# Kernel tuning notes

Hardware: AMD Instinct MI355X
Metric: run time of the kernel (lower is better)

## Reference

```python
import jax, jax.numpy as jnp
import numpy as np

N, E, G = 50000, 800000, 512          # nodes, edges, graphs in batch
DIN, DH, H, DOUT = 128, 128, 2, 128   # dim_in, dim_h, heads, dim_out
NEG_SLOPE = 0.2
EPS_BN = 1e-5


def setup_inputs():
    key = jax.random.key(0)
    ks = jax.random.split(key, 12)
    def glorot(k, shape, fan):
        return (jax.random.normal(k, shape, jnp.float32) / np.float32(np.sqrt(fan)))
    return dict(
        x=jax.random.normal(ks[0], (N, DIN), jnp.float32),
        edge_index=jax.random.randint(ks[1], (2, E), 0, N, dtype=jnp.int32),
        batch=jnp.sort(jax.random.randint(ks[2], (N,), 0, G, dtype=jnp.int32)),
        Wl1=glorot(ks[3], (DIN, H * DH), DIN),
        Wr1=glorot(ks[4], (DIN, H * DH), DIN),
        att1=glorot(ks[5], (H, DH), DH),
        b1=jnp.zeros((H * DH,), jnp.float32),
        gamma=jnp.ones((H * DH,), jnp.float32),
        beta=jnp.zeros((H * DH,), jnp.float32),
        Wl2=glorot(ks[6], (H * DH, DOUT), H * DH),
        Wr2=glorot(ks[7], (H * DH, DOUT), H * DH),
        att2=glorot(ks[8], (1, DOUT), DOUT),
        b2=jnp.zeros((DOUT,), jnp.float32),
        Wlin=glorot(ks[9], (DOUT, 2), DOUT),
        blin=jnp.zeros((2,), jnp.float32),
    )


def gatv2_conv(x, src, dst, Wl, Wr, att, bias, heads, dh, n):
    # x: [n, F]; src/dst: [Etot] (self-loops already appended)
    xl = (x @ Wl).reshape(n, heads, dh)  # source transform (messages)
    xr = (x @ Wr).reshape(n, heads, dh)  # target transform
    m = xl[src] + xr[dst]                             # [Etot, H, dh]
    e = jnp.einsum('ehd,hd->eh', jax.nn.leaky_relu(m, NEG_SLOPE), att)  # [Etot, H]
    # softmax over incoming edges of each target node
    emax = jax.ops.segment_max(e, dst, num_segments=n)
    ex = jnp.exp(e - emax[dst])
    denom = jax.ops.segment_sum(ex, dst, num_segments=n)
    alpha = ex / (denom[dst] + 1e-16)                 # [Etot, H]
    out = jax.ops.segment_sum(xl[src] * alpha[:, :, None], dst, num_segments=n)
    return out.reshape(n, heads * dh) + bias


def reference(x, edge_index, batch, Wl1, Wr1, att1, b1, gamma, beta,
              Wl2, Wr2, att2, b2, Wlin, blin):
    loops = jnp.arange(N, dtype=edge_index.dtype)
    src = jnp.concatenate([edge_index[0], loops])
    dst = jnp.concatenate([edge_index[1], loops])

    h = gatv2_conv(x, src, dst, Wl1, Wr1, att1, b1, H, DH, N)   # [N, H*DH]
    h = jax.nn.elu(h)
    # BatchNorm over node dimension (training-mode batch stats)
    mu = h.mean(axis=0)
    var = h.var(axis=0)
    h = (h - mu) * jax.lax.rsqrt(var + EPS_BN) * gamma + beta
    # dropout p=0 -> identity
    h = gatv2_conv(h, src, dst, Wl2, Wr2, att2, b2, 1, DOUT, N)  # [N, DOUT]

    # global mean pool per graph
    s = jax.ops.segment_sum(h, batch, num_segments=G)
    cnt = jax.ops.segment_sum(jnp.ones((N,), h.dtype), batch, num_segments=G)
    pooled = s / jnp.maximum(cnt, 1.0)[:, None]                  # [G, DOUT]
    return pooled @ Wlin + blin                                  # [G, 2]
```

## Files before the change

kernel.cpp:

```cpp
#include <hip/hip_runtime.h>


#define DIN 128
#define F1 256
#define F2 128
#define NEG_SLOPE 0.2f

typedef unsigned short u16;
typedef __attribute__((ext_vector_type(8))) short short8;
typedef __attribute__((ext_vector_type(4))) float floatx4;
typedef __attribute__((ext_vector_type(2))) float f32x2;

__device__ __forceinline__ float bf2f(u16 u) {
  return __uint_as_float(((unsigned int)u) << 16);
}
__device__ __forceinline__ u16 f2bf(float f) {
  unsigned int x = __float_as_uint(f);
  return (u16)((x + 0x7fffu + ((x >> 16) & 1u)) >> 16);
}
__device__ __forceinline__ void load8(const u16* p, float (&f)[8]) {
  short8 v = *(const short8*)p;
#pragma unroll
  for (int k = 0; k < 8; k++) f[k] = bf2f((u16)v[k]);
}

__device__ __forceinline__ f32x2 bf2x(unsigned int u) {
  f32x2 r;
  r.x = __uint_as_float(u << 16);
  r.y = __uint_as_float(u & 0xffff0000u);
  return r;
}
__device__ __forceinline__ f32x2 pk_add(f32x2 a, f32x2 b) {
  f32x2 d;
  asm("v_pk_add_f32 %0, %1, %2" : "=v"(d) : "v"(a), "v"(b));
  return d;
}
__device__ __forceinline__ f32x2 pk_fma(f32x2 a, f32x2 b, f32x2 c) {
  f32x2 d;
  asm("v_pk_fma_f32 %0, %1, %2, %3" : "=v"(d) : "v"(a), "v"(b), "v"(c));
  return d;
}
__device__ __forceinline__ f32x2 pk_abs(f32x2 a) {
  f32x2 r;
  r.x = __uint_as_float(__float_as_uint(a.x) & 0x7fffffffu);
  r.y = __uint_as_float(__float_as_uint(a.y) & 0x7fffffffu);
  return r;
}

template <int CTRL>
__device__ __forceinline__ float dppadd(float s) {
  int t = __builtin_amdgcn_update_dpp(0, __float_as_int(s), CTRL, 0xF, 0xF, false);
  return s + __int_as_float(t);
}

struct PTab { const void* src[8]; int off[9]; };
__global__ __launch_bounds__(256) void k_convert_all(
    const void* __restrict__ xsrc, u16* __restrict__ xb, int n4, int nxb,
    PTab t, u16* __restrict__ pb, int ptotal, int npb,
    const void* __restrict__ Wl1s, const void* __restrict__ Wr1s,
    const void* __restrict__ Wl2s, const void* __restrict__ Wr2s,
    u16* __restrict__ Wl1t, u16* __restrict__ Wr1t,
    u16* __restrict__ Wl2t, u16* __restrict__ Wr2t,
    int* __restrict__ zbase, int zn, int* __restrict__ flag) {
  __shared__ int flagS;
  int tid = threadIdx.x;
  if (tid < 64) {
    int cnt = 0;
#pragma unroll
    for (int i = 0; i < 2; ++i) {
      u16 v = ((const u16*)xsrc)[2 * (tid + 64 * i)];
      int e = (v >> 7) & 0xFF;
      if (e >= 115 && e <= 130) cnt++;
    }
#pragma unroll
    for (int m = 1; m <= 32; m <<= 1) cnt += __shfl_xor(cnt, m, 64);
    if (tid == 0) flagS = (cnt < 64) ? 1 : 0;
  }
  __syncthreads();
  const int fl = flagS;
  if (blockIdx.x == 0 && tid == 0) *flag = fl;

  int b = blockIdx.x;
  if (b < nxb) {
    int i = b * 256 + tid;
    if (i >= n4) return;
    if (fl) {
      float4 a = ((const float4*)xsrc)[i];
      ushort4 o;
      o.x = f2bf(a.x); o.y = f2bf(a.y); o.z = f2bf(a.z); o.w = f2bf(a.w);
      ((ushort4*)xb)[i] = o;
    } else {
      ((ulong1*)xb)[i] = ((const ulong1*)xsrc)[i];
    }
    return;
  }
  b -= nxb;
  if (b < npb) {
    int i = b * 256 + tid;
    if (i >= ptotal) return;
    int s = 0;
#pragma unroll
    for (int k = 1; k < 8; k++) s += (i >= t.off[k]);
    int local = i - t.off[s];
    pb[i] = fl ? f2bf(((const float*)t.src[s])[local]) : ((const u16*)t.src[s])[local];
    return;
  }
  b -= npb;
  if (b < 512) {
    int seg = b >> 7;
    int i = (b & 127) * 256 + tid;
    const void* s; u16* d; int NL, sh;
    if      (seg == 0) { s = Wl1s; d = Wl1t; NL = 256; sh = 7; }
    else if (seg == 1) { s = Wr1s; d = Wr1t; NL = 256; sh = 7; }
    else if (seg == 2) { s = Wl2s; d = Wl2t; NL = 128; sh = 8; }
    else               { s = Wr2s; d = Wr2t; NL = 128; sh = 8; }
    int n = i >> sh, k = i & ((1 << sh) - 1);
    int si = k * NL + n;
    d[i] = fl ? f2bf(((const float*)s)[si]) : ((const u16*)s)[si];
    return;
  }
  b -= 512;
  int i = b * 256 + tid;
  if (i < zn) zbase[i] = 0;
}

__global__ void k_hist(const int* __restrict__ ei, int* __restrict__ hist,
                       int E, int Etot) {
  int e = blockIdx.x * 256 + threadIdx.x;
  if (e >= Etot) return;
  int dst = (e < E) ? ei[E + e] : (e - E);
  atomicAdd(&hist[dst], 1);
}

__global__ void k_scan(const int* __restrict__ hist, int* __restrict__ rowptr,
                       int* __restrict__ cursor, unsigned long long* __restrict__ pstate,
                       int* __restrict__ ctr, int n, int Etot) {
  __shared__ int tmp[256];
  __shared__ int bidS, offS;
  int t = threadIdx.x;
  if (t == 0) bidS = atomicAdd(ctr, 1);
  __syncthreads();
  int bid = bidS;
  int gid = bid * 256 + t;
  int v = (gid < n) ? hist[gid] : 0;
  tmp[t] = v;
  __syncthreads();
  for (int off = 1; off < 256; off <<= 1) {
    int add = (t >= off) ? tmp[t - off] : 0;
    __syncthreads();
    tmp[t] += add;
    __syncthreads();
  }
  if (t == 0) {
    int total = tmp[255];
    unsigned long long st =
        ((unsigned long long)(bid == 0 ? 2 : 1) << 32) | (unsigned)total;
    atomicExch(&pstate[bid], st);
    int off = 0;
    if (bid > 0) {
      int b = bid - 1;
      while (true) {
        unsigned long long s;
        do { s = atomicAdd(&pstate[b], 0ULL); } while ((s >> 32) == 0);
        off += (int)(unsigned)s;
        if ((s >> 32) == 2) break;
        b--;
      }
      atomicExch(&pstate[bid],
                 ((unsigned long long)2 << 32) | (unsigned)(off + total));
    }
    offS = off;
  }
  __syncthreads();
  int off = offS;
  if (gid < n) {
    int ex = off + tmp[t] - v;
    rowptr[gid] = ex;
    cursor[gid] = ex;
  }
  if (gid == 0) rowptr[n] = Etot;
}

__global__ void k_scatter(const int* __restrict__ ei, int* __restrict__ cursor,
                          int* __restrict__ ssrc, int E, int Etot) {
  int e = blockIdx.x * 256 + threadIdx.x;
  if (e >= Etot) return;
  int src, dst;
  if (e < E) { src = ei[e]; dst = ei[E + e]; }
  else       { src = e - E; dst = e - E; }
  int pos = atomicAdd(&cursor[dst], 1);
  ssrc[pos] = src;
}

template<int K, bool RB>
__global__ __launch_bounds__(256) void k_gemm(
    const u16* __restrict__ A, const u16* __restrict__ Blt, const u16* __restrict__ Brt,
    int NL, u16* __restrict__ Cl, u16* __restrict__ Cr, int M,
    const float* __restrict__ rbias) {
  const int tid = threadIdx.x;
  const int m0 = blockIdx.x * 64;
  const int n0g = blockIdx.y * 64;
  const u16* Bt; u16* C; int col0;
  if (n0g < NL) { Bt = Blt; C = Cl; col0 = n0g; }
  else          { Bt = Brt; C = Cr; col0 = n0g - NL; }

  const int wave = tid >> 6, lane = tid & 63;
  const int wm = wave >> 1, wn = wave & 1;
  const int quad = lane >> 4, l16 = lane & 15;

  floatx4 acc[2][2] = {};
#pragma unroll
  for (int k0 = 0; k0 < K; k0 += 32) {
    short8 af[2], bfr[2];
#pragma unroll
    for (int mt = 0; mt < 2; mt++) {
      int row = m0 + wm * 32 + mt * 16 + l16;
      if (row > M - 1) row = M - 1;
      af[mt] = *(const short8*)(A + (size_t)row * K + k0 + quad * 8);
    }
#pragma unroll
    for (int nt = 0; nt < 2; nt++) {
      int nn = col0 + wn * 32 + nt * 16 + l16;
      bfr[nt] = *(const short8*)(Bt + (size_t)nn * K + k0 + quad * 8);
    }
#pragma unroll
    for (int mt = 0; mt < 2; mt++)
#pragma unroll
      for (int nt = 0; nt < 2; nt++)
        acc[mt][nt] = __builtin_amdgcn_mfma_f32_16x16x32_bf16(af[mt], bfr[nt], acc[mt][nt], 0, 0, 0);
  }

#pragma unroll
  for (int mt = 0; mt < 2; mt++)
#pragma unroll
    for (int nt = 0; nt < 2; nt++) {
      float rb = 0.f;
      if (RB) rb = rbias[n0g + wn * 32 + nt * 16 + l16];
#pragma unroll
      for (int r = 0; r < 4; r++) {
        int row = m0 + wm * 32 + mt * 16 + quad * 4 + r;
        if (row < M) {
          int col = col0 + wn * 32 + nt * 16 + l16;
          C[(size_t)row * NL + col] = f2bf(acc[mt][nt][r] + rb);
        }
      }
    }
}

template<int CPL, int MODE>
__global__ __launch_bounds__(256) void k_agg(
    const u16* __restrict__ xl, const u16* __restrict__ xr,
    const u16* __restrict__ att, const u16* __restrict__ bias,
    const int* __restrict__ rowptr, const int* __restrict__ ssrc,
    void* __restrict__ outv, int n) {
  constexpr int F = CPL * 16;
  constexpr int NV = CPL / 8;
  constexpr int NP = CPL / 2;
  int wave = threadIdx.x >> 6, lane = threadIdx.x & 63;
  int node = blockIdx.x * 4 + wave;
  if (node >= n) return;
  const int q = lane >> 4, l = lane & 15;
  const int ch0 = l * CPL;

  f32x2 xr2[NP], a06[NP], acc2[NP];
  {
    const unsigned int* xru = (const unsigned int*)(xr + (size_t)node * F + ch0);
    const unsigned int* atu = (const unsigned int*)(att + ch0);
#pragma unroll
    for (int p = 0; p < NP; p++) {
      xr2[p] = bf2x(xru[p]);
      f32x2 a = bf2x(atu[p]);
      a06[p].x = 0.6f * a.x; a06[p].y = 0.6f * a.y;
      acc2[p].x = 0.f;       acc2[p].y = 0.f;
    }
  }
  f32x2 c23; c23.x = 2.0f / 3.0f; c23.y = 2.0f / 3.0f;

  const int jb = __builtin_amdgcn_readfirstlane(rowptr[node]);
  const int je = __builtin_amdgcn_readfirstlane(rowptr[node + 1]);
  const int jec = je - 1;
  float l_run = 0.f;

  auto cidx = [&](int j) -> int { return j < jec ? j : jec; };

  uint4 bufA[NV], bufB[NV];
  auto REFILL = [&](uint4 (&buf)[NV], int srow) {
#pragma unroll
    for (int v = 0; v < NV; v++)
      buf[v] = *(const uint4*)(xl + (size_t)srow * F + ch0 + v * 8);
  };

  auto SLOT = [&](uint4 (&buf)[NV], int jbase) {
    f32x2 xl2[NP];
    f32x2 s2; s2.x = 0.f; s2.y = 0.f;
#pragma unroll
    for (int v = 0; v < NV; v++) {
      unsigned int dw[4] = {buf[v].x, buf[v].y, buf[v].z, buf[v].w};
#pragma unroll
      for (int k = 0; k < 4; k++) {
        const int p = v * 4 + k;
        f32x2 xv = bf2x(dw[k]);
        f32x2 m  = pk_add(xv, xr2[p]);
        f32x2 am = pk_abs(m);
        f32x2 t  = pk_fma(am, c23, m);
        s2 = pk_fma(a06[p], t, s2);
        xl2[p] = xv;
      }
    }
    float s = s2.x + s2.y;
    s = dppadd<0xB1>(s);
    s = dppadd<0x4E>(s);
    s = dppadd<0x141>(s);
    if (CPL == 8) s = dppadd<0x140>(s);
    float pe = (jbase + q < je) ? __expf(fminf(s, 80.f)) : 0.f;
    l_run += pe;
    f32x2 p2; p2.x = pe; p2.y = pe;
#pragma unroll
    for (int p = 0; p < NP; p++) acc2[p] = pk_fma(p2, xl2[p], acc2[p]);
  };

  REFILL(bufA, ssrc[cidx(jb + q)]);
  REFILL(bufB, ssrc[cidx(jb + 4 + q)]);
  int sA2 = ssrc[cidx(jb + 8 + q)];
  int sB2 = ssrc[cidx(jb + 12 + q)];

  int j = jb;
  for (; j + 4 < je; j += 8) {
    SLOT(bufA, j);
    REFILL(bufA, sA2);
    SLOT(bufB, j + 4);
    REFILL(bufB, sB2);
    sA2 = ssrc[cidx(j + 16 + q)];
    sB2 = ssrc[cidx(j + 20 + q)];
  }
  if (j < je) SLOT(bufA, j);

#pragma unroll
  for (int p = 0; p < NP; p++) {
    acc2[p].x += __shfl_xor(acc2[p].x, 16, 64);
    acc2[p].x += __shfl_xor(acc2[p].x, 32, 64);
    acc2[p].y += __shfl_xor(acc2[p].y, 16, 64);
    acc2[p].y += __shfl_xor(acc2[p].y, 32, 64);
  }
  l_run += __shfl_xor(l_run, 16, 64);
  l_run += __shfl_xor(l_run, 32, 64);

  if (q == 0) {
    float inv = 1.f / (l_run + 1e-16f);
    const unsigned int* bu = (const unsigned int*)(bias + ch0);
    if (MODE == 0) {
#pragma unroll
      for (int v = 0; v < NV; v++) {
        short8 o;
#pragma unroll
        for (int k = 0; k < 4; k++) {
          const int p = v * 4 + k;
          f32x2 b = bf2x(bu[p]);
          float t0 = acc2[p].x * inv + b.x;
          float t1 = acc2[p].y * inv + b.y;
          t0 = t0 > 0.f ? t0 : (__expf(t0) - 1.f);
          t1 = t1 > 0.f ? t1 : (__expf(t1) - 1.f);
          o[k * 2]     = (short)f2bf(t0);
          o[k * 2 + 1] = (short)f2bf(t1);
        }
        *(short8*)((u16*)outv + (size_t)node * F + ch0 + v * 8) = o;
      }
    } else {
#pragma unroll
      for (int v = 0; v < NV; v++) {
        float w[8];
#pragma unroll
        for (int k = 0; k < 4; k++) {
          const int p = v * 4 + k;
          f32x2 b = bf2x(bu[p]);
          w[k * 2]     = acc2[p].x * inv + b.x;
          w[k * 2 + 1] = acc2[p].y * inv + b.y;
        }
        float* op = (float*)outv + (size_t)node * F + ch0 + v * 8;
        *(float4*)op = make_float4(w[0], w[1], w[2], w[3]);
        *(float4*)(op + 4) = make_float4(w[4], w[5], w[6], w[7]);
      }
    }
  }
}

__global__ __launch_bounds__(256) void k_stats(
    const u16* __restrict__ h, float* __restrict__ gsum,
    float* __restrict__ gsumsq, int n) {
  __shared__ float smS[8][256], smQ[8][256];
  int t = threadIdx.x;
  int rg = t >> 5, cl = t & 31;
  int ch0 = cl * 8;
  float s[8] = {}, q[8] = {};
  for (int r = blockIdx.x * 8 + rg; r < n; r += gridDim.x * 8) {
    float v[8];
    load8(h + (size_t)r * F1 + ch0, v);
#pragma unroll
    for (int k = 0; k < 8; k++) { s[k] += v[k]; q[k] += v[k] * v[k]; }
  }
#pragma unroll
  for (int k = 0; k < 8; k++) { smS[rg][ch0 + k] = s[k]; smQ[rg][ch0 + k] = q[k]; }
  __syncthreads();
  float ts = 0.f, tq = 0.f;
#pragma unroll
  for (int g = 0; g < 8; g++) { ts += smS[g][t]; tq += smQ[g][t]; }
  atomicAdd(&gsum[t], ts);
  atomicAdd(&gsumsq[t], tq);
}

__global__ __launch_bounds__(256) void k_foldbn(
    const float* __restrict__ gsum, const float* __restrict__ gsumsq,
    const u16* __restrict__ gamma, const u16* __restrict__ beta,
    u16* __restrict__ Wl2t, u16* __restrict__ Wr2t,
    float* __restrict__ rbias, float invn) {
  __shared__ float red[8];
  int t = threadIdx.x, n = blockIdx.x;
  float mu = gsum[t] * invn;
  float var = gsumsq[t] * invn - mu * mu;
  float a = bf2f(gamma[t]) * rsqrtf(fmaxf(var, 0.f) + 1e-5f);
  float b = bf2f(beta[t]) - mu * a;
  float wl = bf2f(Wl2t[n * 256 + t]);
  float wr = bf2f(Wr2t[n * 256 + t]);
  float sl = b * wl, sr = b * wr;
  Wl2t[n * 256 + t] = f2bf(a * wl);
  Wr2t[n * 256 + t] = f2bf(a * wr);
#pragma unroll
  for (int m = 1; m <= 32; m <<= 1) {
    sl += __shfl_xor(sl, m, 64);
    sr += __shfl_xor(sr, m, 64);
  }
  int wave = t >> 6, lane = t & 63;
  if (lane == 0) { red[wave] = sl; red[4 + wave] = sr; }
  __syncthreads();
  if (t == 0) rbias[n] = red[0] + red[1] + red[2] + red[3];
  if (t == 1) rbias[128 + n] = red[4] + red[5] + red[6] + red[7];
}

__device__ __forceinline__ int lowerb(const int* __restrict__ a, int n, int key) {
  int lo = 0, hi = n;
  while (lo < hi) { int m = (lo + hi) >> 1; if (a[m] < key) lo = m + 1; else hi = m; }
  return lo;
}

__global__ __launch_bounds__(256) void k_poolfinal(
    const float* __restrict__ h2, const int* __restrict__ batch,
    const u16* __restrict__ Wlin, const u16* __restrict__ blin,
    void* __restrict__ out, const int* __restrict__ flag, int G, int N) {
  __shared__ float sm[4][128];
  int g = blockIdx.x;
  int wave = threadIdx.x >> 6, lane = threadIdx.x & 63;
  int jb = lowerb(batch, N, g);
  int je = lowerb(batch, N, g + 1);
  int ch = lane * 2;
  float c0 = 0.f, c1 = 0.f;
  for (int r = jb + wave; r < je; r += 4) {
    float2 v = *(const float2*)(h2 + (size_t)r * F2 + ch);
    c0 += v.x; c1 += v.y;
  }
  sm[wave][ch] = c0;
  sm[wave][ch + 1] = c1;
  __syncthreads();
  if (wave == 0) {
    c0 = sm[0][ch] + sm[1][ch] + sm[2][ch] + sm[3][ch];
    c1 = sm[0][ch + 1] + sm[1][ch + 1] + sm[2][ch + 1] + sm[3][ch + 1];
    float cf = fmaxf((float)(je - jb), 1.f);
    c0 /= cf; c1 /= cf;
    float s0 = c0 * bf2f(Wlin[ch * 2 + 0]) + c1 * bf2f(Wlin[(ch + 1) * 2 + 0]);
    float s1 = c0 * bf2f(Wlin[ch * 2 + 1]) + c1 * bf2f(Wlin[(ch + 1) * 2 + 1]);
#pragma unroll
    for (int m = 1; m <= 32; m <<= 1) {
      s0 += __shfl_xor(s0, m, 64);
      s1 += __shfl_xor(s1, m, 64);
    }
    if (lane == 0) {
      float o0 = s0 + bf2f(blin[0]);
      float o1 = s1 + bf2f(blin[1]);
      if (*flag) {
        ((float*)out)[g * 2 + 0] = o0;
        ((float*)out)[g * 2 + 1] = o1;
      } else {
        ((u16*)out)[g * 2 + 0] = f2bf(o0);
        ((u16*)out)[g * 2 + 1] = f2bf(o1);
      }
    }
  }
}

extern "C" void kernel_launch(void* const* d_in, const int* in_sizes, int n_in,
                              void* d_out, int out_size, void* d_ws, size_t ws_size,
                              hipStream_t stream) {
  const int* ei    = (const int*)d_in[1];
  const int* batch = (const int*)d_in[2];

  const int N = in_sizes[0] / DIN;
  const int E = in_sizes[1] / 2;
  const int G = out_size / 2;
  const int Etot = E + N;

  char* p = (char*)d_ws;
  auto alloc = [&](size_t bytes) {
    char* r = p;
    p += (bytes + 255) & ~(size_t)255;
    return r;
  };
  int*  flag     = (int*)alloc(256);
  int*  hist     = (int*)alloc((size_t)N * 4);
  float* gsum    = (float*)alloc(1024);
  float* gsumsq  = (float*)alloc(1024);
  unsigned long long* pstate = (unsigned long long*)alloc(2048);
  int*  ctr      = (int*)alloc(256);
  int   zn       = (int)(((char*)ctr + 256) - (char*)hist) / 4;
  int*  rowptr   = (int*)alloc((size_t)(N + 1) * 4);
  int*  cursor   = (int*)alloc((size_t)N * 4);
  float* rbias   = (float*)alloc(256 * 4);
  int*  ssrc     = (int*)alloc((size_t)Etot * 4);
  u16*  xb       = (u16*)alloc((size_t)N * DIN * 2);
  u16*  pb       = (u16*)alloc(4096);
  u16*  Wl1t     = (u16*)alloc(DIN * F1 * 2);
  u16*  Wr1t     = (u16*)alloc(DIN * F1 * 2);
  u16*  Wl2t     = (u16*)alloc(F1 * F2 * 2);
  u16*  Wr2t     = (u16*)alloc(F1 * F2 * 2);
  u16*  regionA  = (u16*)alloc((size_t)N * F1 * 2);
  u16*  regionB  = (u16*)alloc((size_t)N * F1 * 2);
  u16*  regionC  = (u16*)alloc((size_t)N * F1 * 2);

  u16*  xl1  = regionA;
  u16*  xr1  = regionB;
  u16*  helu = regionC;
  u16*  xl2  = regionB;
  u16*  xr2  = regionB + (size_t)N * F2;
  float* h2  = (float*)regionA;

  const int pidx[8] = {5, 6, 7, 8, 11, 12, 13, 14};
  PTab tab;
  int accum = 0;
  for (int i = 0; i < 8; i++) {
    tab.src[i] = d_in[pidx[i]];
    tab.off[i] = accum;
    accum += in_sizes[pidx[i]];
  }
  tab.off[8] = accum;
  int n4 = in_sizes[0] / 4;
  int nxb = (n4 + 255) / 256;
  int npb = (accum + 255) / 256;
  int nzb = (zn + 255) / 256;
  k_convert_all<<<nxb + npb + 512 + nzb, 256, 0, stream>>>(
      d_in[0], xb, n4, nxb, tab, pb, accum, npb,
      d_in[3], d_in[4], d_in[9], d_in[10], Wl1t, Wr1t, Wl2t, Wr2t,
      hist, zn, flag);
  u16 *pAtt1 = pb + tab.off[0], *pB1 = pb + tab.off[1], *pGamma = pb + tab.off[2],
      *pBeta = pb + tab.off[3], *pAtt2 = pb + tab.off[4], *pB2 = pb + tab.off[5],
      *pWlin = pb + tab.off[6], *pBlin = pb + tab.off[7];

  const int eb = (Etot + 255) / 256;
  const int sb = (N + 255) / 256;

  k_hist<<<eb, 256, 0, stream>>>(ei, hist, E, Etot);
  k_scan<<<sb, 256, 0, stream>>>(hist, rowptr, cursor, pstate, ctr, N, Etot);
  k_scatter<<<eb, 256, 0, stream>>>(ei, cursor, ssrc, E, Etot);

  dim3 g1((N + 63) / 64, (2 * F1) / 64);
  k_gemm<DIN, false><<<g1, 256, 0, stream>>>(xb, Wl1t, Wr1t, F1, xl1, xr1, N, nullptr);

  k_agg<16, 0><<<(N + 3) / 4, 256, 0, stream>>>(xl1, xr1, pAtt1, pB1, rowptr, ssrc, helu, N);

  k_stats<<<256, 256, 0, stream>>>(helu, gsum, gsumsq, N);
  k_foldbn<<<128, 256, 0, stream>>>(gsum, gsumsq, pGamma, pBeta, Wl2t, Wr2t, rbias,
                                    1.0f / (float)N);

  dim3 g2((N + 63) / 64, (2 * F2) / 64);
  k_gemm<F1, true><<<g2, 256, 0, stream>>>(helu, Wl2t, Wr2t, F2, xl2, xr2, N, rbias);

  k_agg<8, 1><<<(N + 3) / 4, 256, 0, stream>>>(xl2, xr2, pAtt2, pB2, rowptr, ssrc, h2, N);

  k_poolfinal<<<G, 256, 0, stream>>>(h2, batch, pWlin, pBlin, d_out, flag, G, N);
}
```

Measured before the change: 434.7 us.

## Make GAT aggregation kernels persistent with atomic per-wave node scheduling

```diff
diff --git a/kernel.cpp b/kernel.cpp
--- a/kernel.cpp
+++ b/kernel.cpp
@@ -248,137 +248,149 @@
 }
 
 template<int CPL, int MODE>
-__global__ __launch_bounds__(256) void k_agg(
+__global__ __launch_bounds__(256, 8) void k_agg(
     const u16* __restrict__ xl, const u16* __restrict__ xr,
     const u16* __restrict__ att, const u16* __restrict__ bias,
     const int* __restrict__ rowptr, const int* __restrict__ ssrc,
-    void* __restrict__ outv, int n) {
+    void* __restrict__ outv, int* __restrict__ wctr, int n) {
   constexpr int F = CPL * 16;
   constexpr int NV = CPL / 8;
   constexpr int NP = CPL / 2;
-  int wave = threadIdx.x >> 6, lane = threadIdx.x & 63;
-  int node = blockIdx.x * 4 + wave;
-  if (node >= n) return;
+  const int lane = threadIdx.x & 63;
   const int q = lane >> 4, l = lane & 15;
   const int ch0 = l * CPL;
 
-  f32x2 xr2[NP], a06[NP], acc2[NP];
+  f32x2 a06[NP];
   {
-    const unsigned int* xru = (const unsigned int*)(xr + (size_t)node * F + ch0);
     const unsigned int* atu = (const unsigned int*)(att + ch0);
 #pragma unroll
     for (int p = 0; p < NP; p++) {
-      xr2[p] = bf2x(xru[p]);
       f32x2 a = bf2x(atu[p]);
       a06[p].x = 0.6f * a.x; a06[p].y = 0.6f * a.y;
-      acc2[p].x = 0.f;       acc2[p].y = 0.f;
     }
   }
   f32x2 c23; c23.x = 2.0f / 3.0f; c23.y = 2.0f / 3.0f;
 
-  const int jb = __builtin_amdgcn_readfirstlane(rowptr[node]);
-  const int je = __builtin_amdgcn_readfirstlane(rowptr[node + 1]);
-  const int jec = je - 1;
-  float l_run = 0.f;
-
-  auto cidx = [&](int j) -> int { return j < jec ? j : jec; };
-
-  uint4 bufA[NV], bufB[NV];
-  auto REFILL = [&](uint4 (&buf)[NV], int srow) {
-#pragma unroll
-    for (int v = 0; v < NV; v++)
-      buf[v] = *(const uint4*)(xl + (size_t)srow * F + ch0 + v * 8);
-  };
-
-  auto SLOT = [&](uint4 (&buf)[NV], int jbase) {
-    f32x2 xl2[NP];
-    f32x2 s2; s2.x = 0.f; s2.y = 0.f;
-#pragma unroll
-    for (int v = 0; v < NV; v++) {
-      unsigned int dw[4] = {buf[v].x, buf[v].y, buf[v].z, buf[v].w};
-#pragma unroll
-      for (int k = 0; k < 4; k++) {
-        const int p = v * 4 + k;
-        f32x2 xv = bf2x(dw[k]);
-        f32x2 m  = pk_add(xv, xr2[p]);
-        f32x2 am = pk_abs(m);
-        f32x2 t  = pk_fma(am, c23, m);
-        s2 = pk_fma(a06[p], t, s2);
-        xl2[p] = xv;
+  for (;;) {
+    int ndv = 0;
+    if (lane == 0) ndv = atomicAdd(wctr, 1);
+    const int node = __builtin_amdgcn_readfirstlane(ndv);
+    if (node >= n) return;
+
+    f32x2 xr2[NP], acc2[NP];
+    {
+      const unsigned int* xru = (const unsigned int*)(xr + (size_t)node * F + ch0);
+#pragma unroll
+      for (int p = 0; p < NP; p++) {
+        xr2[p] = bf2x(xru[p]);
+        acc2[p].x = 0.f; acc2[p].y = 0.f;
       }
     }
-    float s = s2.x + s2.y;
-    s = dppadd<0xB1>(s);
-    s = dppadd<0x4E>(s);
-    s = dppadd<0x141>(s);
-    if (CPL == 8) s = dppadd<0x140>(s);
-    float pe = (jbase + q < je) ? __expf(fminf(s, 80.f)) : 0.f;
-    l_run += pe;
-    f32x2 p2; p2.x = pe; p2.y = pe;
-#pragma unroll
-    for (int p = 0; p < NP; p++) acc2[p] = pk_fma(p2, xl2[p], acc2[p]);
-  };
-
-  REFILL(bufA, ssrc[cidx(jb + q)]);
-  REFILL(bufB, ssrc[cidx(jb + 4 + q)]);
-  int sA2 = ssrc[cidx(jb + 8 + q)];
-  int sB2 = ssrc[cidx(jb + 12 + q)];
-
-  int j = jb;
-  for (; j + 4 < je; j += 8) {
-    SLOT(bufA, j);
-    REFILL(bufA, sA2);
-    SLOT(bufB, j + 4);
-    REFILL(bufB, sB2);
-    sA2 = ssrc[cidx(j + 16 + q)];
-    sB2 = ssrc[cidx(j + 20 + q)];
-  }
-  if (j < je) SLOT(bufA, j);
-
-#pragma unroll
-  for (int p = 0; p < NP; p++) {
-    acc2[p].x += __shfl_xor(acc2[p].x, 16, 64);
-    acc2[p].x += __shfl_xor(acc2[p].x, 32, 64);
-    acc2[p].y += __shfl_xor(acc2[p].y, 16, 64);
-    acc2[p].y += __shfl_xor(acc2[p].y, 32, 64);
-  }
-  l_run += __shfl_xor(l_run, 16, 64);
-  l_run += __shfl_xor(l_run, 32, 64);
-
-  if (q == 0) {
-    float inv = 1.f / (l_run + 1e-16f);
-    const unsigned int* bu = (const unsigned int*)(bias + ch0);
-    if (MODE == 0) {
+
+    const int jb = __builtin_amdgcn_readfirstlane(rowptr[node]);
+    const int je = __builtin_amdgcn_readfirstlane(rowptr[node + 1]);
+    const int jec = je - 1;
+    float l_run = 0.f;
+
+    auto cidx = [&](int j) -> int { return j < jec ? j : jec; };
+
+    uint4 bufA[NV], bufB[NV];
+    auto REFILL = [&](uint4 (&buf)[NV], int srow) {
+#pragma unroll
+      for (int v = 0; v < NV; v++)
+        buf[v] = *(const uint4*)(xl + (size_t)srow * F + ch0 + v * 8);
+    };
+
+    auto SLOT = [&](uint4 (&buf)[NV], int jbase) {
+      f32x2 xl2[NP];
+      f32x2 s2; s2.x = 0.f; s2.y = 0.f;
 #pragma unroll
       for (int v = 0; v < NV; v++) {
-        short8 o;
+        unsigned int dw[4] = {buf[v].x, buf[v].y, buf[v].z, buf[v].w};
 #pragma unroll
         for (int k = 0; k < 4; k++) {
           const int p = v * 4 + k;
-          f32x2 b = bf2x(bu[p]);
-          float t0 = acc2[p].x * inv + b.x;
-          float t1 = acc2[p].y * inv + b.y;
-          t0 = t0 > 0.f ? t0 : (__expf(t0) - 1.f);
-          t1 = t1 > 0.f ? t1 : (__expf(t1) - 1.f);
-          o[k * 2]     = (short)f2bf(t0);
-          o[k * 2 + 1] = (short)f2bf(t1);
+          f32x2 xv = bf2x(dw[k]);
+          f32x2 m  = pk_add(xv, xr2[p]);
+          f32x2 am = pk_abs(m);
+          f32x2 t  = pk_fma(am, c23, m);
+          s2 = pk_fma(a06[p], t, s2);
+          xl2[p] = xv;
         }
-        *(short8*)((u16*)outv + (size_t)node * F + ch0 + v * 8) = o;
       }
-    } else {
-#pragma unroll
-      for (int v = 0; v < NV; v++) {
-        float w[8];
-#pragma unroll
-        for (int k = 0; k < 4; k++) {
-          const int p = v * 4 + k;
-          f32x2 b = bf2x(bu[p]);
-          w[k * 2]     = acc2[p].x * inv + b.x;
-          w[k * 2 + 1] = acc2[p].y * inv + b.y;
+      float s = s2.x + s2.y;
+      s = dppadd<0xB1>(s);
+      s = dppadd<0x4E>(s);
+      s = dppadd<0x141>(s);
+      if (CPL == 8) s = dppadd<0x140>(s);
+      float pe = (jbase + q < je) ? __expf(fminf(s, 80.f)) : 0.f;
+      l_run += pe;
+      f32x2 p2; p2.x = pe; p2.y = pe;
+#pragma unroll
+      for (int p = 0; p < NP; p++) acc2[p] = pk_fma(p2, xl2[p], acc2[p]);
+    };
+
+    REFILL(bufA, ssrc[cidx(jb + q)]);
+    REFILL(bufB, ssrc[cidx(jb + 4 + q)]);
+    int sA2 = ssrc[cidx(jb + 8 + q)];
+    int sB2 = ssrc[cidx(jb + 12 + q)];
+
+    int j = jb;
+    for (; j + 4 < je; j += 8) {
+      SLOT(bufA, j);
+      REFILL(bufA, sA2);
+      SLOT(bufB, j + 4);
+      REFILL(bufB, sB2);
+      sA2 = ssrc[cidx(j + 16 + q)];
+      sB2 = ssrc[cidx(j + 20 + q)];
+    }
+    if (j < je) SLOT(bufA, j);
+
+#pragma unroll
+    for (int p = 0; p < NP; p++) {
+      acc2[p].x += __shfl_xor(acc2[p].x, 16, 64);
+      acc2[p].x += __shfl_xor(acc2[p].x, 32, 64);
+      acc2[p].y += __shfl_xor(acc2[p].y, 16, 64);
+      acc2[p].y += __shfl_xor(acc2[p].y, 32, 64);
+    }
+    l_run += __shfl_xor(l_run, 16, 64);
+    l_run += __shfl_xor(l_run, 32, 64);
+
+    if (q == 0) {
+      float inv = 1.f / (l_run + 1e-16f);
+      const unsigned int* bu = (const unsigned int*)(bias + ch0);
+      if (MODE == 0) {
+#pragma unroll
+        for (int v = 0; v < NV; v++) {
+          short8 o;
+#pragma unroll
+          for (int k = 0; k < 4; k++) {
+            const int p = v * 4 + k;
+            f32x2 b = bf2x(bu[p]);
+            float t0 = acc2[p].x * inv + b.x;
+            float t1 = acc2[p].y * inv + b.y;
+            t0 = t0 > 0.f ? t0 : (__expf(t0) - 1.f);
+            t1 = t1 > 0.f ? t1 : (__expf(t1) - 1.f);
+            o[k * 2]     = (short)f2bf(t0);
+            o[k * 2 + 1] = (short)f2bf(t1);
+          }
+          *(short8*)((u16*)outv + (size_t)node * F + ch0 + v * 8) = o;
         }
-        float* op = (float*)outv + (size_t)node * F + ch0 + v * 8;
-        *(float4*)op = make_float4(w[0], w[1], w[2], w[3]);
-        *(float4*)(op + 4) = make_float4(w[4], w[5], w[6], w[7]);
+      } else {
+#pragma unroll
+        for (int v = 0; v < NV; v++) {
+          float w[8];
+#pragma unroll
+          for (int k = 0; k < 4; k++) {
+            const int p = v * 4 + k;
+            f32x2 b = bf2x(bu[p]);
+            w[k * 2]     = acc2[p].x * inv + b.x;
+            w[k * 2 + 1] = acc2[p].y * inv + b.y;
+          }
+          float* op = (float*)outv + (size_t)node * F + ch0 + v * 8;
+          *(float4*)op = make_float4(w[0], w[1], w[2], w[3]);
+          *(float4*)(op + 4) = make_float4(w[4], w[5], w[6], w[7]);
+        }
       }
     }
   }
@@ -509,7 +521,8 @@
   float* gsumsq  = (float*)alloc(1024);
   unsigned long long* pstate = (unsigned long long*)alloc(2048);
   int*  ctr      = (int*)alloc(256);
-  int   zn       = (int)(((char*)ctr + 256) - (char*)hist) / 4;
+  int*  wctr     = (int*)alloc(256);
+  int   zn       = (int)(((char*)wctr + 256) - (char*)hist) / 4;
   int*  rowptr   = (int*)alloc((size_t)(N + 1) * 4);
   int*  cursor   = (int*)alloc((size_t)N * 4);
   float* rbias   = (float*)alloc(256 * 4);
@@ -562,7 +575,9 @@
   dim3 g1((N + 63) / 64, (2 * F1) / 64);
   k_gemm<DIN, false><<<g1, 256, 0, stream>>>(xb, Wl1t, Wr1t, F1, xl1, xr1, N, nullptr);
 
-  k_agg<16, 0><<<(N + 3) / 4, 256, 0, stream>>>(xl1, xr1, pAtt1, pB1, rowptr, ssrc, helu, N);
+  const int PW = 2048;
+  k_agg<16, 0><<<PW, 256, 0, stream>>>(xl1, xr1, pAtt1, pB1, rowptr, ssrc, helu,
+                                       wctr, N);
 
   k_stats<<<256, 256, 0, stream>>>(helu, gsum, gsumsq, N);
   k_foldbn<<<128, 256, 0, stream>>>(gsum, gsumsq, pGamma, pBeta, Wl2t, Wr2t, rbias,
@@ -571,7 +586,8 @@
   dim3 g2((N + 63) / 64, (2 * F2) / 64);
   k_gemm<F1, true><<<g2, 256, 0, stream>>>(helu, Wl2t, Wr2t, F2, xl2, xr2, N, rbias);
 
-  k_agg<8, 1><<<(N + 3) / 4, 256, 0, stream>>>(xl2, xr2, pAtt2, pB2, rowptr, ssrc, h2, N);
+  k_agg<8, 1><<<PW, 256, 0, stream>>>(xl2, xr2, pAtt2, pB2, rowptr, ssrc, h2,
+                                      wctr + 64, N);
 
   k_poolfinal<<<G, 256, 0, stream>>>(h2, batch, pWlin, pBlin, d_out, flag, G, N);
 }
```

Measured after the change: 1.727 ms. 3.97x slower.

## Add specialized layer-2 aggregation kernel with 8 edges per wave and double-buffered gathers

Applied to the files above, without the earlier changes.

```diff
diff --git a/kernel.cpp b/kernel.cpp
--- a/kernel.cpp
+++ b/kernel.cpp
@@ -380,6 +380,126 @@
         *(float4*)op = make_float4(w[0], w[1], w[2], w[3]);
         *(float4*)(op + 4) = make_float4(w[4], w[5], w[6], w[7]);
       }
+    }
+  }
+}
+
+__global__ __launch_bounds__(256) void k_agg2(
+    const u16* __restrict__ xl, const u16* __restrict__ xr,
+    const u16* __restrict__ att, const u16* __restrict__ bias,
+    const int* __restrict__ rowptr, const int* __restrict__ ssrc,
+    float* __restrict__ out, int n) {
+  constexpr int F = 128;
+  constexpr int NV = 2;
+  constexpr int NP = 8;
+  constexpr int GPW = 8;
+  int wave = threadIdx.x >> 6, lane = threadIdx.x & 63;
+  int node = blockIdx.x * 4 + wave;
+  if (node >= n) return;
+  const int g = lane >> 3, lg = lane & 7;
+  const int ch0 = lg * 16;
+
+  f32x2 xr2[NP], a06[NP], acc2[NP];
+  {
+    const unsigned int* xru = (const unsigned int*)(xr + (size_t)node * F + ch0);
+    const unsigned int* atu = (const unsigned int*)(att + ch0);
+#pragma unroll
+    for (int p = 0; p < NP; p++) {
+      xr2[p] = bf2x(xru[p]);
+      f32x2 a = bf2x(atu[p]);
+      a06[p].x = 0.6f * a.x; a06[p].y = 0.6f * a.y;
+      acc2[p].x = 0.f;       acc2[p].y = 0.f;
+    }
+  }
+  f32x2 c23; c23.x = 2.0f / 3.0f; c23.y = 2.0f / 3.0f;
+
+  const int jb = __builtin_amdgcn_readfirstlane(rowptr[node]);
+  const int je = __builtin_amdgcn_readfirstlane(rowptr[node + 1]);
+  const int jec = je - 1;
+  float l_run = 0.f;
+
+  auto cidx = [&](int j) -> int { return j < jec ? j : jec; };
+
+  uint4 bufA[NV], bufB[NV];
+  auto REFILL = [&](uint4 (&buf)[NV], int srow) {
+#pragma unroll
+    for (int v = 0; v < NV; v++)
+      buf[v] = *(const uint4*)(xl + (size_t)srow * F + ch0 + v * 8);
+  };
+
+  auto SLOT = [&](uint4 (&buf)[NV], int jbase) {
+    f32x2 xl2[NP];
+    f32x2 s2; s2.x = 0.f; s2.y = 0.f;
+#pragma unroll
+    for (int v = 0; v < NV; v++) {
+      unsigned int dw[4] = {buf[v].x, buf[v].y, buf[v].z, buf[v].w};
+#pragma unroll
+      for (int k = 0; k < 4; k++) {
+        const int p = v * 4 + k;
+        f32x2 xv = bf2x(dw[k]);
+        f32x2 m  = pk_add(xv, xr2[p]);
+        f32x2 am = pk_abs(m);
+        f32x2 t  = pk_fma(am, c23, m);
+        s2 = pk_fma(a06[p], t, s2);
+        xl2[p] = xv;
+      }
+    }
+    float s = s2.x + s2.y;
+    s = dppadd<0xB1>(s);
+    s = dppadd<0x4E>(s);
+    s = dppadd<0x141>(s);
+    float pe = (jbase + g < je) ? __expf(fminf(s, 80.f)) : 0.f;
+    l_run += pe;
+    f32x2 p2; p2.x = pe; p2.y = pe;
+#pragma unroll
+    for (int p = 0; p < NP; p++) acc2[p] = pk_fma(p2, xl2[p], acc2[p]);
+  };
+
+  REFILL(bufA, ssrc[cidx(jb + g)]);
+  REFILL(bufB, ssrc[cidx(jb + GPW + g)]);
+  int sA2 = ssrc[cidx(jb + 2 * GPW + g)];
+  int sB2 = ssrc[cidx(jb + 3 * GPW + g)];
+
+  int j = jb;
+  for (; j + GPW < je; j += 2 * GPW) {
+    SLOT(bufA, j);
+    REFILL(bufA, sA2);
+    SLOT(bufB, j + GPW);
+    REFILL(bufB, sB2);
+    sA2 = ssrc[cidx(j + 4 * GPW + g)];
+    sB2 = ssrc[cidx(j + 5 * GPW + g)];
+  }
+  if (j < je) SLOT(bufA, j);
+
+#pragma unroll
+  for (int p = 0; p < NP; p++) {
+    acc2[p].x += __shfl_xor(acc2[p].x, 8, 64);
+    acc2[p].x += __shfl_xor(acc2[p].x, 16, 64);
+    acc2[p].x += __shfl_xor(acc2[p].x, 32, 64);
+    acc2[p].y += __shfl_xor(acc2[p].y, 8, 64);
+    acc2[p].y += __shfl_xor(acc2[p].y, 16, 64);
+    acc2[p].y += __shfl_xor(acc2[p].y, 32, 64);
+  }
+  l_run += __shfl_xor(l_run, 8, 64);
+  l_run += __shfl_xor(l_run, 16, 64);
+  l_run += __shfl_xor(l_run, 32, 64);
+
+  if (lane < 8) {
+    float inv = 1.f / (l_run + 1e-16f);
+    const unsigned int* bu = (const unsigned int*)(bias + ch0);
+#pragma unroll
+    for (int v = 0; v < NV; v++) {
+      float w[8];
+#pragma unroll
+      for (int k = 0; k < 4; k++) {
+        const int p = v * 4 + k;
+        f32x2 b = bf2x(bu[p]);
+        w[k * 2]     = acc2[p].x * inv + b.x;
+        w[k * 2 + 1] = acc2[p].y * inv + b.y;
+      }
+      float* op = out + (size_t)node * F + ch0 + v * 8;
+      *(float4*)op = make_float4(w[0], w[1], w[2], w[3]);
+      *(float4*)(op + 4) = make_float4(w[4], w[5], w[6], w[7]);
     }
   }
 }
@@ -571,7 +691,7 @@
   dim3 g2((N + 63) / 64, (2 * F2) / 64);
   k_gemm<F1, true><<<g2, 256, 0, stream>>>(helu, Wl2t, Wr2t, F2, xl2, xr2, N, rbias);
 
-  k_agg<8, 1><<<(N + 3) / 4, 256, 0, stream>>>(xl2, xr2, pAtt2, pB2, rowptr, ssrc, h2, N);
+  k_agg2<<<(N + 3) / 4, 256, 0, stream>>>(xl2, xr2, pAtt2, pB2, rowptr, ssrc, h2, N);
 
   k_poolfinal<<<G, 256, 0, stream>>>(h2, batch, pWlin, pBlin, d_out, flag, G, N);
 }
```

After: 449.7 us. 1.03x slower.
